# Kernel optimization log

Hardware: AMD Instinct MI355X
Metric: run time of the kernel (lower is better)

The kernel has to match this reference:

```python
import jax, jax.numpy as jnp
import numpy as np

N = 50000
E = 600000
HID = 128
NF = 128
NG = 50
CUTOFF = 10.0
LOG2 = float(np.log(2.0))


def ssp(x):
    # shifted softplus: softplus(x) - log(2)
    return jax.nn.softplus(x) - LOG2


def setup_inputs() -> dict:
    key = jax.random.key(0)
    ks = jax.random.split(key, 12)
    h = jax.random.normal(ks[0], (N, HID), dtype=jnp.float32)
    edge_index = jax.random.randint(ks[1], (2, E), 0, N)
    edge_weight = jax.random.uniform(ks[2], (E,), dtype=jnp.float32) * CUTOFF
    edge_attr = jax.random.normal(ks[3], (E, NG), dtype=jnp.float32)
    # parameters (torch Linear weight layout: [out, in])
    def xavier(k, shape):
        fan_out, fan_in = shape
        lim = np.sqrt(6.0 / (fan_in + fan_out))
        return jax.random.uniform(k, shape, jnp.float32, -lim, lim)
    mlp_w0 = xavier(ks[4], (NF, NG))
    mlp_b0 = jnp.zeros((NF,), jnp.float32)
    mlp_w2 = xavier(ks[5], (NF, NF))
    mlp_b2 = jnp.zeros((NF,), jnp.float32)
    lin1_w = xavier(ks[6], (NF, HID))
    lin2_w = xavier(ks[7], (HID, NF))
    lin2_b = jnp.zeros((HID,), jnp.float32)
    lin_w = xavier(ks[8], (HID, HID))
    lin_b = jnp.zeros((HID,), jnp.float32)
    return {
        "h": h, "edge_index": edge_index, "edge_weight": edge_weight,
        "edge_attr": edge_attr, "mlp_w0": mlp_w0, "mlp_b0": mlp_b0,
        "mlp_w2": mlp_w2, "mlp_b2": mlp_b2, "lin1_w": lin1_w,
        "lin2_w": lin2_w, "lin2_b": lin2_b, "lin_w": lin_w, "lin_b": lin_b,
    }


def reference(h, edge_index, edge_weight, edge_attr, mlp_w0, mlp_b0,
              mlp_w2, mlp_b2, lin1_w, lin2_w, lin2_b, lin_w, lin_b):
    src, dst = edge_index[0], edge_index[1]
    # CFConv
    h1 = h @ lin1_w.T                                   # [N, NF]
    c = 0.5 * (jnp.cos(edge_weight / CUTOFF * jnp.pi) + 1.0)  # [E]
    W = ssp(edge_attr @ mlp_w0.T + mlp_b0) @ mlp_w2.T + mlp_b2  # [E, NF]
    message = c[:, None] * (W * h1[src])                # [E, NF]
    agg = jax.ops.segment_sum(message, dst, num_segments=h.shape[0])
    h2 = (h1 + agg) @ lin2_w.T + lin2_b                 # [N, HID]
    # InteractionBlock tail
    return ssp(h2) @ lin_w.T + lin_b
```

## Files before the change

### kernel.cpp

```cpp
#include <hip/hip_runtime.h>
#include <math.h>

#define HID 128
#define NF  128
#define NG  50

typedef unsigned short ushort_t;
typedef unsigned short us8 __attribute__((ext_vector_type(8)));
typedef unsigned short us4 __attribute__((ext_vector_type(4)));
typedef unsigned short us2 __attribute__((ext_vector_type(2)));
typedef __bf16 bf16x8 __attribute__((ext_vector_type(8)));
typedef float f32x4 __attribute__((ext_vector_type(4)));

__device__ inline float ssp_fast(float x) {
    float t = __builtin_amdgcn_exp2f(fabsf(x) * -1.4426950408889634f);
    float l = __builtin_amdgcn_logf(1.0f + t);
    return fmaxf(x, 0.0f) + 0.6931471805599453f * (l - 1.0f);
}

__device__ inline ushort_t f2bf(float f) {
    return __builtin_bit_cast(ushort_t, (__bf16)f);
}
__device__ inline float bf2f(ushort_t h) {
    unsigned u = ((unsigned)h) << 16;
    return __builtin_bit_cast(float, u);
}

__device__ inline void gload16(const void* g, void* l) {
    __builtin_amdgcn_global_load_lds(
        (const __attribute__((address_space(1))) void*)g,
        (__attribute__((address_space(3))) void*)l, 16, 0, 0);
}

__global__ void prep_count(const int* __restrict__ dstI, int* counts,
                           int* __restrict__ slot,
                           const float* __restrict__ lin1_w,
                           const float* __restrict__ lin2_w,
                           const float* __restrict__ lin_w,
                           const float* __restrict__ mlp_w0,
                           const float* __restrict__ mlp_w2,
                           ushort_t* __restrict__ l1b,
                           ushort_t* __restrict__ l2b,
                           ushort_t* __restrict__ lfb,
                           ushort_t* __restrict__ w0g,
                           ushort_t* __restrict__ w2g,
                           int* __restrict__ sidecar_pad,
                           int E, int nsp) {
    int idx = blockIdx.x * 256 + threadIdx.x;
    if (idx < E) {
        slot[idx] = atomicAdd(&counts[dstI[idx]], 1);
        return;
    }
    int k = idx - E;
    if (k < 49152) {
        int m = k >> 14, i = k & 16383;
        int o = i >> 7, kk = i & 127;
        const float* s = (m == 0) ? lin1_w : (m == 1) ? lin2_w : lin_w;
        ushort_t*    d = (m == 0) ? l1b    : (m == 1) ? l2b    : lfb;
        d[o * 128 + (kk ^ ((o & 7) << 3))] = f2bf(s[i]);
    } else if (k < 57344) {
        int i = k - 49152;
        int o = i >> 6, kk = i & 63;
        float v = (kk < 50) ? mlp_w0[o * 50 + kk] : 0.f;
        w0g[i] = f2bf(v);
    } else if (k < 73728) {
        int i = k - 57344;
        w2g[i] = f2bf(mlp_w2[i]);
    } else if (k < 73728 + nsp) {
        sidecar_pad[k - 73728] = 0;
    }
}

__global__ __launch_bounds__(1024) void scan1(const int* __restrict__ counts,
                                              int* __restrict__ off,
                                              int* __restrict__ bsum, int n) {
    __shared__ int s[1024];
    int t = threadIdx.x, g = blockIdx.x * 1024 + t;
    int c = (g < n) ? counts[g] : 0;
    s[t] = c;
    __syncthreads();
    for (int d = 1; d < 1024; d <<= 1) {
        int v = (t >= d) ? s[t - d] : 0;
        __syncthreads();
        s[t] += v;
        __syncthreads();
    }
    if (g < n) off[g] = s[t] - c;
    if (t == 1023) bsum[blockIdx.x] = s[1023];
}
__global__ void scan2(int* bsum, int nb) {
    __shared__ int s[64];
    int t = threadIdx.x;
    int v = (t < nb) ? bsum[t] : 0;
    s[t] = v;
    __syncthreads();
    for (int d = 1; d < 64; d <<= 1) {
        int u = (t >= d) ? s[t - d] : 0;
        __syncthreads();
        s[t] += u;
        __syncthreads();
    }
    if (t < nb) bsum[t] = s[t] - v;
}

__global__ __launch_bounds__(256) void permute_lite(
    const int* __restrict__ srcI, const int* __restrict__ dstI,
    const int* __restrict__ slot, const int* __restrict__ off,
    const int* __restrict__ bsum, const float* __restrict__ ew,
    int4* __restrict__ sidecar, int E)
{
    int e = blockIdx.x * 256 + threadIdx.x;
    if (e >= E) return;
    int d = dstI[e];
    int p = off[d] + bsum[d >> 10] + slot[e];
    float cw = 0.5f * (__builtin_amdgcn_cosf(ew[e] * 0.05f) + 1.0f);
    sidecar[p] = make_int4(srcI[e], d, __float_as_int(cw), e);
}

__global__ __launch_bounds__(1024, 4) void gemm_h1(
    const float* __restrict__ A, const ushort_t* __restrict__ Wb,
    ushort_t* __restrict__ h1b, float* __restrict__ aggz, int n_rows)
{
    __shared__ ushort_t a_s[128 * 128];
    __shared__ ushort_t w_s[128 * 128];
    const int tid = threadIdx.x;
    const int n0 = blockIdx.x * 128;
    const int lane = tid & 63, wid = tid >> 6;

    #pragma unroll
    for (int i = 0; i < 2; ++i) {
        int cid = wid * 2 + i;
        gload16(Wb + cid * 512 + lane * 8, w_s + cid * 512);
    }
    {
        int r = tid >> 3, q = tid & 7;
        int n = n0 + r;
        float vals[16];
        if (n < n_rows) {
            #pragma unroll
            for (int j = 0; j < 4; ++j) {
                f32x4 v = ((const f32x4*)A)[(size_t)n * 32 + q * 4 + j];
                #pragma unroll
                for (int x = 0; x < 4; ++x) vals[j * 4 + x] = v[x];
            }
        } else {
            #pragma unroll
            for (int x = 0; x < 16; ++x) vals[x] = 0.f;
        }
        int sw = (r & 7) << 3;
        #pragma unroll
        for (int hh = 0; hh < 2; ++hh) {
            us8 pk;
            #pragma unroll
            for (int x = 0; x < 8; ++x) pk[x] = f2bf(vals[hh * 8 + x]);
            *(us8*)&a_s[r * 128 + ((q * 16 + hh * 8) ^ sw)] = pk;
        }
    }
    __syncthreads();

    const int og = (wid >> 2) * 32;
    const int rg = (wid & 3) * 32;
    const int lm = lane & 15, lh = lane >> 4;

    f32x4 acc[2][2];
    #pragma unroll
    for (int mt = 0; mt < 2; ++mt)
        #pragma unroll
        for (int nt = 0; nt < 2; ++nt) acc[mt][nt] = (f32x4){0.f, 0.f, 0.f, 0.f};

    #pragma unroll
    for (int ks = 0; ks < 4; ++ks) {
        int k8 = ks * 32 + lh * 8;
        bf16x8 af[2], wf[2];
        #pragma unroll
        for (int mt = 0; mt < 2; ++mt) {
            int m = rg + mt * 16 + lm;
            af[mt] = __builtin_bit_cast(bf16x8,
                *(const us8*)&a_s[m * 128 + (k8 ^ ((m & 7) << 3))]);
        }
        #pragma unroll
        for (int nt = 0; nt < 2; ++nt) {
            int n = og + nt * 16 + lm;
            wf[nt] = __builtin_bit_cast(bf16x8,
                *(const us8*)&w_s[n * 128 + (k8 ^ ((n & 7) << 3))]);
        }
        #pragma unroll
        for (int mt = 0; mt < 2; ++mt)
            #pragma unroll
            for (int nt = 0; nt < 2; ++nt)
                acc[mt][nt] = __builtin_amdgcn_mfma_f32_16x16x32_bf16(
                    af[mt], wf[nt], acc[mt][nt], 0, 0, 0);
    }

    #pragma unroll
    for (int nt = 0; nt < 2; ++nt) {
        int outc = og + nt * 16 + lm;
        #pragma unroll
        for (int mt = 0; mt < 2; ++mt) {
            int rbase = rg + mt * 16 + lh * 4;
            #pragma unroll
            for (int j = 0; j < 4; ++j) {
                int n = n0 + rbase + j;
                if (n < n_rows) {
                    h1b[(size_t)n * 128 + outc] = f2bf(acc[mt][nt][j]);
                    aggz[(size_t)n * 128 + outc] = 0.f;
                }
            }
        }
    }
}

__global__ __launch_bounds__(1024, 4) void gemm23_fused(
    const ushort_t* __restrict__ h1b, const float* __restrict__ agg,
    const ushort_t* __restrict__ l2b, const float* __restrict__ b2,
    const ushort_t* __restrict__ lfb, const float* __restrict__ lb,
    float* __restrict__ outF, int n_rows)
{
    __shared__ ushort_t a_s[128 * 128];
    __shared__ ushort_t w_s[128 * 128];
    const int tid = threadIdx.x;
    const int n0 = blockIdx.x * 128;
    const int lane = tid & 63, wid = tid >> 6;

    #pragma unroll
    for (int i = 0; i < 2; ++i) {
        int cid = wid * 2 + i;
        gload16(l2b + cid * 512 + lane * 8, w_s + cid * 512);
    }
    {
        int r = tid >> 3, q = tid & 7;
        int n = n0 + r;
        float vals[16];
        if (n < n_rows) {
            us8 hb0 = *(const us8*)&h1b[(size_t)n * 128 + q * 16];
            us8 hb1 = *(const us8*)&h1b[(size_t)n * 128 + q * 16 + 8];
            #pragma unroll
            for (int j = 0; j < 4; ++j) {
                f32x4 av = ((const f32x4*)agg)[(size_t)n * 32 + q * 4 + j];
                #pragma unroll
                for (int x = 0; x < 4; ++x) {
                    int c = j * 4 + x;
                    float hv = bf2f(c < 8 ? hb0[c] : hb1[c - 8]);
                    vals[c] = hv + av[x];
                }
            }
        } else {
            #pragma unroll
            for (int x = 0; x < 16; ++x) vals[x] = 0.f;
        }
        int sw = (r & 7) << 3;
        #pragma unroll
        for (int hh = 0; hh < 2; ++hh) {
            us8 pk;
            #pragma unroll
            for (int x = 0; x < 8; ++x) pk[x] = f2bf(vals[hh * 8 + x]);
            *(us8*)&a_s[r * 128 + ((q * 16 + hh * 8) ^ sw)] = pk;
        }
    }
    __syncthreads();

    const int og = (wid >> 2) * 32;
    const int rg = (wid & 3) * 32;
    const int lm = lane & 15, lh = lane >> 4;

    f32x4 acc[2][2];
    #pragma unroll
    for (int mt = 0; mt < 2; ++mt)
        #pragma unroll
        for (int nt = 0; nt < 2; ++nt) acc[mt][nt] = (f32x4){0.f, 0.f, 0.f, 0.f};
    #pragma unroll
    for (int ks = 0; ks < 4; ++ks) {
        int k8 = ks * 32 + lh * 8;
        bf16x8 af[2], wf[2];
        #pragma unroll
        for (int mt = 0; mt < 2; ++mt) {
            int m = rg + mt * 16 + lm;
            af[mt] = __builtin_bit_cast(bf16x8,
                *(const us8*)&a_s[m * 128 + (k8 ^ ((m & 7) << 3))]);
        }
        #pragma unroll
        for (int nt = 0; nt < 2; ++nt) {
            int n = og + nt * 16 + lm;
            wf[nt] = __builtin_bit_cast(bf16x8,
                *(const us8*)&w_s[n * 128 + (k8 ^ ((n & 7) << 3))]);
        }
        #pragma unroll
        for (int mt = 0; mt < 2; ++mt)
            #pragma unroll
            for (int nt = 0; nt < 2; ++nt)
                acc[mt][nt] = __builtin_amdgcn_mfma_f32_16x16x32_bf16(
                    af[mt], wf[nt], acc[mt][nt], 0, 0, 0);
    }
    __syncthreads();

    #pragma unroll
    for (int i = 0; i < 2; ++i) {
        int cid = wid * 2 + i;
        gload16(lfb + cid * 512 + lane * 8, w_s + cid * 512);
    }
    #pragma unroll
    for (int nt = 0; nt < 2; ++nt) {
        int outc = og + nt * 16 + lm;
        float bv = b2[outc];
        #pragma unroll
        for (int mt = 0; mt < 2; ++mt) {
            int rbase = rg + mt * 16 + lh * 4;
            #pragma unroll
            for (int j = 0; j < 4; ++j) {
                int r = rbase + j;
                a_s[r * 128 + (outc ^ ((r & 7) << 3))] =
                    f2bf(ssp_fast(acc[mt][nt][j] + bv));
            }
        }
    }
    __syncthreads();

    f32x4 acc2[2][2];
    #pragma unroll
    for (int mt = 0; mt < 2; ++mt)
        #pragma unroll
        for (int nt = 0; nt < 2; ++nt) acc2[mt][nt] = (f32x4){0.f, 0.f, 0.f, 0.f};
    #pragma unroll
    for (int ks = 0; ks < 4; ++ks) {
        int k8 = ks * 32 + lh * 8;
        bf16x8 af[2], wf[2];
        #pragma unroll
        for (int mt = 0; mt < 2; ++mt) {
            int m = rg + mt * 16 + lm;
            af[mt] = __builtin_bit_cast(bf16x8,
                *(const us8*)&a_s[m * 128 + (k8 ^ ((m & 7) << 3))]);
        }
        #pragma unroll
        for (int nt = 0; nt < 2; ++nt) {
            int n = og + nt * 16 + lm;
            wf[nt] = __builtin_bit_cast(bf16x8,
                *(const us8*)&w_s[n * 128 + (k8 ^ ((n & 7) << 3))]);
        }
        #pragma unroll
        for (int mt = 0; mt < 2; ++mt)
            #pragma unroll
            for (int nt = 0; nt < 2; ++nt)
                acc2[mt][nt] = __builtin_amdgcn_mfma_f32_16x16x32_bf16(
                    af[mt], wf[nt], acc2[mt][nt], 0, 0, 0);
    }

    #pragma unroll
    for (int nt = 0; nt < 2; ++nt) {
        int outc = og + nt * 16 + lm;
        float bv = lb[outc];
        #pragma unroll
        for (int mt = 0; mt < 2; ++mt) {
            int rbase = rg + mt * 16 + lh * 4;
            #pragma unroll
            for (int j = 0; j < 4; ++j) {
                int n = n0 + rbase + j;
                if (n < n_rows)
                    outF[(size_t)n * 128 + outc] = acc2[mt][nt][j] + bv;
            }
        }
    }
}

__global__ __launch_bounds__(512, 6) void edge_fused(
    const float* __restrict__ ea, const int4* __restrict__ sidecar,
    const ushort_t* __restrict__ w0g, const ushort_t* __restrict__ w2g,
    const float* __restrict__ b0g, const float* __restrict__ b2g,
    const ushort_t* __restrict__ h1b, float* __restrict__ agg, int E)
{
    __shared__ __align__(16) char blob[50688];
    ushort_t* ea_s = (ushort_t*)blob;
    ushort_t* u_s  = (ushort_t*)(blob + 16384);
    ushort_t* m_sb = (ushort_t*)blob;
    float* cws = (float*)(blob + 49152);
    int* srcs  = (int*)(blob + 49664);
    int* dsts  = (int*)(blob + 50176);

    const int tid = threadIdx.x;
    const int p0 = blockIdx.x * 128;
    const int lane = tid & 63, wid = tid >> 6;
    const int out0w = (wid >> 1) * 32;
    const int e0w   = (wid & 1) * 64;
    const int lm = lane & 15, lh = lane >> 4;

    {
        int r = tid >> 2, q = tid & 3;
        int p = p0 + r;
        int eidx = (p < E) ? ((const int*)sidecar)[(size_t)p * 4 + 3] : 0;
        const float2* row2 = (const float2*)(ea + (size_t)eidx * 50);
        us8 pk0 = {0, 0, 0, 0, 0, 0, 0, 0};
        us8 pk1 = {0, 0, 0, 0, 0, 0, 0, 0};
        if (q < 3) {
            #pragma unroll
            for (int j = 0; j < 4; ++j) {
                float2 f = row2[q * 8 + j];
                pk0[2 * j]     = f2bf(f.x);
                pk0[2 * j + 1] = f2bf(f.y);
            }
            #pragma unroll
            for (int j = 0; j < 4; ++j) {
                float2 f = row2[q * 8 + 4 + j];
                pk1[2 * j]     = f2bf(f.x);
                pk1[2 * j + 1] = f2bf(f.y);
            }
        } else {
            float2 f = row2[24];
            pk0[0] = f2bf(f.x);
            pk0[1] = f2bf(f.y);
        }
        int sw = (r & 7) << 3;
        *(us8*)&ea_s[r * 64 + ((q * 16)     ^ sw)] = pk0;
        *(us8*)&ea_s[r * 64 + ((q * 16 + 8) ^ sw)] = pk1;
    }
    if (tid < 128) {
        int4 sc = sidecar[p0 + tid];
        srcs[tid] = sc.x; dsts[tid] = sc.y; cws[tid] = __int_as_float(sc.z);
    }

    bf16x8 w0f[2][2];
    #pragma unroll
    for (int ks = 0; ks < 2; ++ks)
        #pragma unroll
        for (int mt = 0; mt < 2; ++mt) {
            int n = out0w + mt * 16 + lm;
            w0f[ks][mt] = __builtin_bit_cast(bf16x8,
                *(const us8*)&w0g[n * 64 + ks * 32 + lh * 8]);
        }
    __syncthreads();

    f32x4 acc1[2][4];
    #pragma unroll
    for (int mt = 0; mt < 2; ++mt)
        #pragma unroll
        for (int nt = 0; nt < 4; ++nt) acc1[mt][nt] = (f32x4){0.f, 0.f, 0.f, 0.f};
    #pragma unroll
    for (int ks = 0; ks < 2; ++ks) {
        int k8 = ks * 32 + lh * 8;
        #pragma unroll
        for (int nt = 0; nt < 4; ++nt) {
            int e = e0w + nt * 16 + lm;
            bf16x8 be = __builtin_bit_cast(bf16x8,
                *(const us8*)&ea_s[e * 64 + (k8 ^ ((e & 7) << 3))]);
            #pragma unroll
            for (int mt = 0; mt < 2; ++mt)
                acc1[mt][nt] = __builtin_amdgcn_mfma_f32_16x16x32_bf16(
                    w0f[ks][mt], be, acc1[mt][nt], 0, 0, 0);
        }
    }

    #pragma unroll
    for (int mt = 0; mt < 2; ++mt) {
        int out0 = out0w + mt * 16 + lh * 4;
        f32x4 b0v = *(const f32x4*)&b0g[out0];
        #pragma unroll
        for (int nt = 0; nt < 4; ++nt) {
            int e = e0w + nt * 16 + lm;
            us4 pk;
            #pragma unroll
            for (int j = 0; j < 4; ++j)
                pk[j] = f2bf(ssp_fast(acc1[mt][nt][j] + b0v[j]));
            *(us4*)&u_s[e * 128 + (out0 ^ ((e & 7) << 3))] = pk;
        }
    }

    bf16x8 w2f[4][2];
    #pragma unroll
    for (int ks = 0; ks < 4; ++ks)
        #pragma unroll
        for (int mt = 0; mt < 2; ++mt) {
            int n = out0w + mt * 16 + lm;
            w2f[ks][mt] = __builtin_bit_cast(bf16x8,
                *(const us8*)&w2g[n * 128 + ks * 32 + lh * 8]);
        }
    __syncthreads();

    f32x4 acc2[2][4];
    #pragma unroll
    for (int mt = 0; mt < 2; ++mt)
        #pragma unroll
        for (int nt = 0; nt < 4; ++nt) acc2[mt][nt] = (f32x4){0.f, 0.f, 0.f, 0.f};
    #pragma unroll
    for (int ks = 0; ks < 4; ++ks) {
        int k8 = ks * 32 + lh * 8;
        #pragma unroll
        for (int nt = 0; nt < 4; ++nt) {
            int e = e0w + nt * 16 + lm;
            bf16x8 be = __builtin_bit_cast(bf16x8,
                *(const us8*)&u_s[e * 128 + (k8 ^ ((e & 7) << 3))]);
            #pragma unroll
            for (int mt = 0; mt < 2; ++mt)
                acc2[mt][nt] = __builtin_amdgcn_mfma_f32_16x16x32_bf16(
                    w2f[ks][mt], be, acc2[mt][nt], 0, 0, 0);
        }
    }
    __syncthreads();

    #pragma unroll
    for (int mt = 0; mt < 2; ++mt) {
        int out0 = out0w + mt * 16 + lh * 4;
        f32x4 b2v = *(const f32x4*)&b2g[out0];
        #pragma unroll
        for (int nt = 0; nt < 4; ++nt) {
            int e = e0w + nt * 16 + lm;
            float cvv = cws[e];
            us4 pk;
            #pragma unroll
            for (int j = 0; j < 4; ++j)
                pk[j] = f2bf(cvv * (acc2[mt][nt][j] + b2v[j]));
            *(us4*)&m_sb[e * 128 + (out0 ^ ((e & 7) << 2))] = pk;
        }
    }
    __syncthreads();

    {
        const int i0 = wid * 16;
        const int cp = lane;
        us2 h1r[16];
        #pragma unroll
        for (int j = 0; j < 16; ++j) {
            int s = srcs[i0 + j];
            h1r[j] = *(const us2*)&h1b[(size_t)s * 128 + cp * 2];
        }
        float sx = 0.f, sy = 0.f;
        int prev = dsts[i0];
        #pragma unroll
        for (int j = 0; j < 16; ++j) {
            int i = i0 + j;
            int d = dsts[i];
            us2 wv = *(const us2*)&m_sb[i * 128 + ((cp * 2) ^ ((i & 7) << 2))];
            if (d != prev) {
                atomicAdd(&agg[(size_t)prev * 128 + cp * 2], sx);
                atomicAdd(&agg[(size_t)prev * 128 + cp * 2 + 1], sy);
                sx = 0.f; sy = 0.f; prev = d;
            }
            sx += bf2f(wv[0]) * bf2f(h1r[j][0]);
            sy += bf2f(wv[1]) * bf2f(h1r[j][1]);
        }
        atomicAdd(&agg[(size_t)prev * 128 + cp * 2], sx);
        atomicAdd(&agg[(size_t)prev * 128 + cp * 2 + 1], sy);
    }
}

extern "C" void kernel_launch(void* const* d_in, const int* in_sizes, int n_in,
                              void* d_out, int out_size, void* d_ws, size_t ws_size,
                              hipStream_t stream) {
    const float* h       = (const float*)d_in[0];
    const int*   ei      = (const int*)  d_in[1];
    const float* ew      = (const float*)d_in[2];
    const float* ea      = (const float*)d_in[3];
    const float* mlp_w0  = (const float*)d_in[4];
    const float* mlp_b0  = (const float*)d_in[5];
    const float* mlp_w2  = (const float*)d_in[6];
    const float* mlp_b2  = (const float*)d_in[7];
    const float* lin1_w  = (const float*)d_in[8];
    const float* lin2_w  = (const float*)d_in[9];
    const float* lin2_b  = (const float*)d_in[10];
    const float* lin_w   = (const float*)d_in[11];
    const float* lin_b   = (const float*)d_in[12];
    float* out = (float*)d_out;
    float* ws  = (float*)d_ws;

    const int N = in_sizes[0] / HID;
    const int E = in_sizes[2];
    const int PADE = (E + 127) & ~127;
    const int NODE_PAD = (N + 256) & ~255;
    const int NSB = (N + 1023) / 1024;

    float* agg   = ws;
    ushort_t* h1b = (ushort_t*)(agg + (size_t)N * 128);
    ushort_t* l1b = (ushort_t*)((float*)h1b + (size_t)N * 64);
    ushort_t* l2b = l1b + 16384;
    ushort_t* lfb = l2b + 16384;
    ushort_t* w0g = lfb + 16384;
    ushort_t* w2g = w0g + 8192;
    int* counts  = (int*)(w2g + 16384);
    int* off     = counts + NODE_PAD;
    int* bsum    = off + NODE_PAD;
    int* slot    = bsum + 64;
    int4* sidecar = (int4*)(slot + E);

    const int* srcI = ei;
    const int* dstI = ei + E;

    hipMemsetAsync(counts, 0, (size_t)NODE_PAD * 4, stream);

    const int nsp = (PADE - E) * 4;
    int total_threads = E + 73728 + nsp;
    prep_count<<<(total_threads + 255) / 256, 256, 0, stream>>>(
        dstI, counts, slot, lin1_w, lin2_w, lin_w, mlp_w0, mlp_w2,
        l1b, l2b, lfb, w0g, w2g, (int*)(sidecar + E), E, nsp);

    scan1<<<NSB, 1024, 0, stream>>>(counts, off, bsum, N);
    scan2<<<1, 64, 0, stream>>>(bsum, NSB);

    permute_lite<<<(E + 255) / 256, 256, 0, stream>>>(
        srcI, dstI, slot, off, bsum, ew, sidecar, E);

    int ngrid = (N + 127) / 128;
    gemm_h1<<<ngrid, 1024, 0, stream>>>(h, l1b, h1b, agg, N);

    edge_fused<<<PADE / 128, 512, 0, stream>>>(ea, sidecar, w0g, w2g,
                                               mlp_b0, mlp_b2, h1b, agg, E);

    gemm23_fused<<<ngrid, 1024, 0, stream>>>(h1b, agg, l2b, lin2_b,
                                             lfb, lin_b, out, N);
}
```

Before: 179.3 us.

## Merge scan2 and permute into h1 GEMM launch as extra blocks

Removes the separate scan2 and permute_lite launches. The final block-sum scan is now recomputed redundantly in each of a set of extra blocks appended to the h1 GEMM grid, and those blocks then perform the edge permutation. This cuts two kernel launches and lets the permute run alongside the GEMM blocks. The h1 gather loads in edge_fused are also hoisted above a __syncthreads so their latency overlaps the barrier. In exchange, every permute block repeats the small 64-entry scan, and permute blocks now run at 1024 threads with the GEMM's large shared-memory footprint, which may lower occupancy.

```diff
diff --git a/kernel.cpp b/kernel.cpp
--- a/kernel.cpp
+++ b/kernel.cpp
@@ -88,42 +88,48 @@
     if (g < n) off[g] = s[t] - c;
     if (t == 1023) bsum[blockIdx.x] = s[1023];
 }
-__global__ void scan2(int* bsum, int nb) {
-    __shared__ int s[64];
-    int t = threadIdx.x;
-    int v = (t < nb) ? bsum[t] : 0;
-    s[t] = v;
-    __syncthreads();
-    for (int d = 1; d < 64; d <<= 1) {
-        int u = (t >= d) ? s[t - d] : 0;
-        __syncthreads();
-        s[t] += u;
-        __syncthreads();
-    }
-    if (t < nb) bsum[t] = s[t] - v;
-}
-
-__global__ __launch_bounds__(256) void permute_lite(
+
+__global__ __launch_bounds__(1024, 4) void h1_and_permute(
+    const float* __restrict__ A, const ushort_t* __restrict__ Wb,
+    ushort_t* __restrict__ h1b, float* __restrict__ aggz, int n_rows, int ngrid,
     const int* __restrict__ srcI, const int* __restrict__ dstI,
     const int* __restrict__ slot, const int* __restrict__ off,
-    const int* __restrict__ bsum, const float* __restrict__ ew,
+    const int* __restrict__ bsum, int nsb, const float* __restrict__ ew,
     int4* __restrict__ sidecar, int E)
-{
-    int e = blockIdx.x * 256 + threadIdx.x;
-    if (e >= E) return;
-    int d = dstI[e];
-    int p = off[d] + bsum[d >> 10] + slot[e];
-    float cw = 0.5f * (__builtin_amdgcn_cosf(ew[e] * 0.05f) + 1.0f);
-    sidecar[p] = make_int4(srcI[e], d, __float_as_int(cw), e);
-}
-
-__global__ __launch_bounds__(1024, 4) void gemm_h1(
-    const float* __restrict__ A, const ushort_t* __restrict__ Wb,
-    ushort_t* __restrict__ h1b, float* __restrict__ aggz, int n_rows)
 {
     __shared__ ushort_t a_s[128 * 128];
     __shared__ ushort_t w_s[128 * 128];
     const int tid = threadIdx.x;
+
+    if (blockIdx.x >= ngrid) {
+        int* cs  = (int*)a_s;
+        int* cse = (int*)a_s + 64;
+        int own = 0;
+        if (tid < 64) {
+            own = (tid < nsb) ? bsum[tid] : 0;
+            cs[tid] = own;
+        }
+        __syncthreads();
+        for (int d = 1; d < 64; d <<= 1) {
+            int v = 0;
+            if (tid < 64 && tid >= d) v = cs[tid - d];
+            __syncthreads();
+            if (tid < 64) cs[tid] += v;
+            __syncthreads();
+        }
+        if (tid < 64) cse[tid] = cs[tid] - own;
+        __syncthreads();
+
+        int e = (blockIdx.x - ngrid) * 1024 + tid;
+        if (e < E) {
+            int d = dstI[e];
+            int p = off[d] + cse[d >> 10] + slot[e];
+            float cw = 0.5f * (__builtin_amdgcn_cosf(ew[e] * 0.05f) + 1.0f);
+            sidecar[p] = make_int4(srcI[e], d, __float_as_int(cw), e);
+        }
+        return;
+    }
+
     const int n0 = blockIdx.x * 128;
     const int lane = tid & 63, wid = tid >> 6;
 
@@ -509,17 +515,18 @@
             *(us4*)&m_sb[e * 128 + (out0 ^ ((e & 7) << 2))] = pk;
         }
     }
+
+    const int i0 = wid * 16;
+    us2 h1r[16];
+    #pragma unroll
+    for (int j = 0; j < 16; ++j) {
+        int s = srcs[i0 + j];
+        h1r[j] = *(const us2*)&h1b[(size_t)s * 128 + lane * 2];
+    }
     __syncthreads();
 
     {
-        const int i0 = wid * 16;
         const int cp = lane;
-        us2 h1r[16];
-        #pragma unroll
-        for (int j = 0; j < 16; ++j) {
-            int s = srcs[i0 + j];
-            h1r[j] = *(const us2*)&h1b[(size_t)s * 128 + cp * 2];
-        }
         float sx = 0.f, sy = 0.f;
         int prev = dsts[i0];
         #pragma unroll
@@ -590,13 +597,12 @@
         l1b, l2b, lfb, w0g, w2g, (int*)(sidecar + E), E, nsp);
 
     scan1<<<NSB, 1024, 0, stream>>>(counts, off, bsum, N);
-    scan2<<<1, 64, 0, stream>>>(bsum, NSB);
-
-    permute_lite<<<(E + 255) / 256, 256, 0, stream>>>(
-        srcI, dstI, slot, off, bsum, ew, sidecar, E);
 
     int ngrid = (N + 127) / 128;
-    gemm_h1<<<ngrid, 1024, 0, stream>>>(h, l1b, h1b, agg, N);
+    int pb    = (E + 1023) / 1024;
+    h1_and_permute<<<ngrid + pb, 1024, 0, stream>>>(
+        h, l1b, h1b, agg, N, ngrid,
+        srcI, dstI, slot, off, bsum, NSB, ew, sidecar, E);
 
     edge_fused<<<PADE / 128, 512, 0, stream>>>(ea, sidecar, w0g, w2g,
                                                mlp_b0, mlp_b2, h1b, agg, E);
```

Result: no change. 180.1 us (+0.4%).
